# Kernel optimization log

Hardware: AMD Instinct MI355X
Metric: run time of the kernel (lower is better)

Reference implementation:

```python
import jax, jax.numpy as jnp
import numpy as np

EPS = 1e-5
N_P = 16


def _bn(x, g, b):
    # BatchNorm1d in training mode: batch stats over (batch, points), biased var
    m = jnp.mean(x, axis=(0, 2), keepdims=True)
    v = jnp.var(x, axis=(0, 2), keepdims=True)
    return g[None, :, None] * (x - m) * jax.lax.rsqrt(v + EPS) + b[None, :, None]


def _conv1x1(w, b, x):
    # w: [out, in], x: [B, in, N]
    return jnp.einsum('oc,bcn->bon', w, x) + b[None, :, None]


def setup_inputs() -> dict:
    key = jax.random.key(0)
    ks = iter(jax.random.split(key, 40))
    B, N = 16, 16384

    def conv_p(o, i):
        w = jax.random.normal(next(ks), (o, i), jnp.float32) * (1.0 / np.sqrt(i))
        b = jax.random.normal(next(ks), (o,), jnp.float32) * 0.02
        return w, b

    def bn_p(c):
        g = jnp.ones((c,), jnp.float32) + jax.random.normal(next(ks), (c,), jnp.float32) * 0.02
        b = jax.random.normal(next(ks), (c,), jnp.float32) * 0.02
        return g, b

    inp = {}
    inp['x'] = jax.random.normal(next(ks), (B, 4, N), jnp.float32)
    inp['w1'], inp['b1'] = conv_p(64, 4)
    inp['g1'], inp['be1'] = bn_p(64)
    inp['w2'], inp['b2'] = conv_p(128, 64)
    inp['g2'], inp['be2'] = bn_p(128)
    inp['w3'], inp['b3'] = conv_p(32, 128)
    inp['g3'], inp['be3'] = bn_p(32)
    # conv9: Conv2d(32, 1, kernel=(1, N_P)) -> store as [32, N_P] + scalar bias
    inp['w9'] = jax.random.normal(next(ks), (32, N_P), jnp.float32) * (1.0 / np.sqrt(32 * N_P))
    inp['b9'] = jax.random.normal(next(ks), (1,), jnp.float32) * 0.02
    inp['w4'], inp['b4'] = conv_p(512, 96)
    inp['g4'], inp['be4'] = bn_p(512)
    inp['w5'], inp['b5'] = conv_p(256, 512)
    inp['g5'], inp['be5'] = bn_p(256)
    inp['w6'], inp['b6'] = conv_p(128, 256)
    inp['g6'], inp['be6'] = bn_p(128)
    inp['w7'], inp['b7'] = conv_p(3, 128)
    return inp


def reference(x, w1, b1, g1, be1, w2, b2, g2, be2, w3, b3, g3, be3,
              w9, b9, w4, b4, g4, be4, w5, b5, g5, be5, w6, b6, g6, be6, w7, b7):
    B, _, N = x.shape
    h1 = jax.nn.relu(_bn(_conv1x1(w1, b1, x), g1, be1))      # [B,64,N] (pointfeat)
    h2 = jax.nn.relu(_bn(_conv1x1(w2, b2, h1), g2, be2))     # [B,128,N]
    h3 = _bn(_conv1x1(w3, b3, h2), g3, be3)                  # [B,32,N]

    # SoftPool: per key-channel ascending sort of points; only first N_P columns used.
    idxs = jnp.argsort(h3, axis=2)[:, :, :N_P]               # [B,32,N_P]
    # sp[b,c,k,p] = h3[b,c, idxs[b,k,p]]
    sp = jnp.take_along_axis(h3[:, :, None, :], idxs[:, None, :, :], axis=3)  # [B,32,32,N_P]

    # conv9: Conv2d(32->1, kernel (1,N_P)) collapses channel and N_P dims -> [B,32]
    v = jnp.einsum('cp,bckp->bk', w9, sp) + b9               # [B,32]
    glob = jnp.broadcast_to(v[:, :, None], (B, 32, N))       # repeat over points

    h = jnp.concatenate([glob, h1], axis=1)                  # [B,96,N]
    h = jax.nn.relu(_bn(_conv1x1(w4, b4, h), g4, be4))       # [B,512,N]
    h = jax.nn.relu(_bn(_conv1x1(w5, b5, h), g5, be5))       # [B,256,N]
    h = jax.nn.relu(_bn(_conv1x1(w6, b6, h), g6, be6))       # [B,128,N]
    out = jnp.tanh(_conv1x1(w7, b7, h))                      # [B,3,N]
    return out
```

## Files before the change

kernel.cpp:

```cpp
#include <hip/hip_runtime.h>
#include <hip/hip_fp16.h>
#include <math.h>
#include <type_traits>

#define NPTS 16384
#define NB 16
#define BNTOT (NB * NPTS)
#define NP 16

typedef _Float16 f16;
typedef __attribute__((ext_vector_type(8))) _Float16 f16x8;
typedef __attribute__((ext_vector_type(4))) float f32x4;

struct alignas(8) H4 { __half2 a, b; };
struct alignas(8) F16x4 { f16 v[4]; };

template<int CIN, int OT, int MODE, bool TANH_OUT, bool STATS, bool OUTAFF,
         typename TIN, typename TOUT>
__global__ __launch_bounds__(256, 2) void conv_k(
    const TIN* __restrict__ X, const float* __restrict__ vglob,
    const float* __restrict__ W, const float* __restrict__ bias,
    const float* __restrict__ insc, const float* __restrict__ insh,
    const float* __restrict__ outsc, const float* __restrict__ outsh,
    TOUT* __restrict__ Y, float* __restrict__ ssum, float* __restrict__ ssq,
    int COUT)
{
    constexpr int PT = 4;
    constexpr int NT = 256 * PT;
    constexpr int CC = (CIN < 128) ? CIN : 128;
    constexpr int XC = (MODE == 2) ? 64 : CIN;
    __shared__ __align__(16) float Ws[CC][OT];
    __shared__ float lsum[OT];
    __shared__ float lsq[OT];

    const int tid = threadIdx.x;
    const int tile = blockIdx.y;
    const int b = (tile * NT) / NPTS;
    const int n = (tile * NT) % NPTS + tid * PT;
    const int obase = blockIdx.x * OT;

    if (STATS) {
        for (int i = tid; i < OT; i += 256) { lsum[i] = 0.f; lsq[i] = 0.f; }
    }

    float acc[OT][PT];
#pragma unroll
    for (int o = 0; o < OT; ++o)
#pragma unroll
        for (int p = 0; p < PT; ++p) acc[o][p] = 0.f;

    const TIN* Xb = X + (size_t)b * XC * NPTS;

    for (int c0 = 0; c0 < CIN; c0 += CC) {
        for (int i = tid; i < CC * OT; i += 256) {
            int c = i % CC, o = i / CC;
            int oo = obase + o;
            Ws[c][o] = (oo < COUT) ? W[(size_t)oo * CIN + (c0 + c)] : 0.f;
        }
        __syncthreads();
#pragma unroll 2
        for (int c = 0; c < CC; ++c) {
            float xv[PT];
            if (MODE == 2 && (c0 + c) < 32) {
                float gv = vglob[b * 32 + (c0 + c)];
#pragma unroll
                for (int p = 0; p < PT; ++p) xv[p] = gv;
            } else {
                const int cx = (MODE == 2) ? (c0 + c - 32) : (c0 + c);
                if constexpr (std::is_same<TIN, __half>::value) {
                    H4 t = *(const H4*)(Xb + (size_t)cx * NPTS + n);
                    xv[0] = __low2float(t.a); xv[1] = __high2float(t.a);
                    xv[2] = __low2float(t.b); xv[3] = __high2float(t.b);
                } else {
                    float4 t = *(const float4*)(Xb + (size_t)cx * NPTS + n);
                    xv[0] = t.x; xv[1] = t.y; xv[2] = t.z; xv[3] = t.w;
                }
                if (MODE == 1) {
                    float s = insc[cx], h = insh[cx];
#pragma unroll
                    for (int p = 0; p < PT; ++p)
                        xv[p] = fmaxf(fmaf(xv[p], s, h), 0.f);
                }
            }
            const float4* wrow = (const float4*)(&Ws[c][0]);
#pragma unroll
            for (int o4 = 0; o4 < OT / 4; ++o4) {
                float4 w = wrow[o4];
#pragma unroll
                for (int p = 0; p < PT; ++p) {
                    acc[o4 * 4 + 0][p] = fmaf(w.x, xv[p], acc[o4 * 4 + 0][p]);
                    acc[o4 * 4 + 1][p] = fmaf(w.y, xv[p], acc[o4 * 4 + 1][p]);
                    acc[o4 * 4 + 2][p] = fmaf(w.z, xv[p], acc[o4 * 4 + 2][p]);
                    acc[o4 * 4 + 3][p] = fmaf(w.w, xv[p], acc[o4 * 4 + 3][p]);
                }
            }
        }
        __syncthreads();
    }

#pragma unroll
    for (int o = 0; o < OT; ++o) {
        const int oo = obase + o;
        if (oo < COUT) {
            float v[PT];
#pragma unroll
            for (int p = 0; p < PT; ++p) v[p] = acc[o][p];
            if (OUTAFF) {
                float s = outsc[oo], h = outsh[oo];
#pragma unroll
                for (int p = 0; p < PT; ++p) v[p] = fmaxf(fmaf(v[p], s, h), 0.f);
            }
            if (TANH_OUT) {
                float bb = bias[oo];
#pragma unroll
                for (int p = 0; p < PT; ++p) v[p] = tanhf(v[p] + bb);
            }
            const size_t ofs = ((size_t)b * COUT + oo) * NPTS + n;
            if constexpr (std::is_same<TOUT, __half>::value) {
                H4 t; t.a = __floats2half2_rn(v[0], v[1]);
                t.b = __floats2half2_rn(v[2], v[3]);
                *(H4*)(Y + ofs) = t;
            } else {
                *(float4*)(Y + ofs) = make_float4(v[0], v[1], v[2], v[3]);
            }
            if (STATS) {
                float s = v[0] + v[1] + v[2] + v[3];
                float q = fmaf(v[0], v[0], fmaf(v[1], v[1], fmaf(v[2], v[2], v[3] * v[3])));
#pragma unroll
                for (int d = 32; d >= 1; d >>= 1) {
                    s += __shfl_xor(s, d, 64);
                    q += __shfl_xor(q, d, 64);
                }
                if ((tid & 63) == 0) {
                    atomicAdd(&lsum[o], s);
                    atomicAdd(&lsq[o], q);
                }
            }
        }
    }
    if (STATS) {
        __syncthreads();
        for (int i = tid; i < OT; i += 256) {
            int oo = obase + i;
            if (oo < COUT) {
                atomicAdd(&ssum[oo], lsum[i]);
                atomicAdd(&ssq[oo], lsq[i]);
            }
        }
    }
}

__global__ void bnstats_k(const float* __restrict__ ssum, const float* __restrict__ ssq,
                          const float* __restrict__ g, const float* __restrict__ be,
                          float* __restrict__ scale, float* __restrict__ shift, int C)
{
    int c = blockIdx.x * blockDim.x + threadIdx.x;
    if (c >= C) return;
    const float inv = 1.0f / (float)BNTOT;
    float m = ssum[c] * inv;
    float var = fmaf(ssq[c], inv, -m * m);
    float sc = g[c] / sqrtf(var + 1e-5f);
    scale[c] = sc;
    shift[c] = fmaf(-m, sc, be[c]);
}

__global__ __launch_bounds__(256) void softpool_k(
    const float* __restrict__ y3, const float* __restrict__ sc3,
    const float* __restrict__ sh3, const float* __restrict__ w9,
    const float* __restrict__ b9, float* __restrict__ vout)
{
    extern __shared__ float vals[];
    __shared__ int sidx[NP];
    __shared__ float wv[4];
    __shared__ int wi[4];
    __shared__ float ps[4];

    const int tid = threadIdx.x;
    const int b = blockIdx.x >> 5;
    const int k = blockIdx.x & 31;

    const float* src = y3 + ((size_t)b * 32 + k) * NPTS;
    const float sck = sc3[k], shk = sh3[k];
    for (int i = tid; i < NPTS; i += 256) vals[i] = fmaf(src[i], sck, shk);
    __syncthreads();

    for (int p = 0; p < NP; ++p) {
        float bv = INFINITY;
        int bi = 0x7fffffff;
        for (int i = tid; i < NPTS; i += 256) {
            float x = vals[i];
            if (x < bv) { bv = x; bi = i; }
        }
#pragma unroll
        for (int d = 32; d >= 1; d >>= 1) {
            float ov = __shfl_xor(bv, d, 64);
            int oi = __shfl_xor(bi, d, 64);
            if (ov < bv || (ov == bv && oi < bi)) { bv = ov; bi = oi; }
        }
        if ((tid & 63) == 0) { wv[tid >> 6] = bv; wi[tid >> 6] = bi; }
        __syncthreads();
        if (tid == 0) {
            for (int w = 1; w < 4; ++w)
                if (wv[w] < bv || (wv[w] == bv && wi[w] < bi)) { bv = wv[w]; bi = wi[w]; }
            sidx[p] = bi;
            vals[bi] = INFINITY;
        }
        __syncthreads();
    }

    float part = 0.f;
    for (int i = tid; i < 32 * NP; i += 256) {
        int c = i >> 4, p = i & 15;
        float h = fmaf(y3[((size_t)b * 32 + c) * NPTS + sidx[p]], sc3[c], sh3[c]);
        part += w9[c * NP + p] * h;
    }
#pragma unroll
    for (int d = 32; d >= 1; d >>= 1) part += __shfl_xor(part, d, 64);
    if ((tid & 63) == 0) ps[tid >> 6] = part;
    __syncthreads();
    if (tid == 0) vout[b * 32 + k] = ps[0] + ps[1] + ps[2] + ps[3] + b9[0];
}

__global__ __launch_bounds__(256) void transformT_k(
    const float* __restrict__ y1, const float* __restrict__ sc,
    const float* __restrict__ sh, f16* __restrict__ h1T, float* __restrict__ S1b)
{
    __shared__ float arr[64][65];
    __shared__ float s1loc[64];
    const int tid = threadIdx.x;
    const int b = blockIdx.x >> 8;
    const int n0 = (blockIdx.x & 255) * 64;
    if (tid < 64) s1loc[tid] = 0.f;

    const int c = tid >> 2, j4 = tid & 3;
    const float scv = sc[c], shv = sh[c];
    const float* src = y1 + ((size_t)b * 64 + c) * NPTS + n0 + j4 * 16;
    float ls = 0.f;
#pragma unroll
    for (int j = 0; j < 4; ++j) {
        float4 v = *(const float4*)(src + j * 4);
        float r0 = fmaxf(fmaf(v.x, scv, shv), 0.f);
        float r1 = fmaxf(fmaf(v.y, scv, shv), 0.f);
        float r2 = fmaxf(fmaf(v.z, scv, shv), 0.f);
        float r3 = fmaxf(fmaf(v.w, scv, shv), 0.f);
        arr[j4 * 16 + j * 4 + 0][c] = r0;
        arr[j4 * 16 + j * 4 + 1][c] = r1;
        arr[j4 * 16 + j * 4 + 2][c] = r2;
        arr[j4 * 16 + j * 4 + 3][c] = r3;
        ls += (r0 + r1) + (r2 + r3);
    }
    ls += __shfl_xor(ls, 1, 64);
    ls += __shfl_xor(ls, 2, 64);
    if (j4 == 0) atomicAdd(&s1loc[c], ls);
    __syncthreads();

    const int n = tid >> 2, cj = (tid & 3) * 16;
    f16x8 h0, h1v;
#pragma unroll
    for (int jj = 0; jj < 8; ++jj) h0[jj] = (f16)arr[n][cj + jj];
#pragma unroll
    for (int jj = 0; jj < 8; ++jj) h1v[jj] = (f16)arr[n][cj + 8 + jj];
    f16* dst = h1T + ((size_t)b * NPTS + n0 + n) * 64 + cj;
    *(f16x8*)(dst) = h0;
    *(f16x8*)(dst + 8) = h1v;

    if (tid < 64) atomicAdd(&S1b[b * 64 + tid], s1loc[tid]);
}

__global__ __launch_bounds__(256, 2) void msyrk_k(const f16* __restrict__ h1T,
                                                  float* __restrict__ M)
{
    __shared__ float Mlds[4][4096];
    const int tid = threadIdx.x;
    const int lane = tid & 63;
    const int llo = lane & 15, lhi = lane >> 4;
    const int wv = tid >> 6;
    const int gw = blockIdx.x * 4 + wv;
    constexpr int SPW = (BNTOT / 32) / 2048;

    f32x4 acc[4][4];
#pragma unroll
    for (int ti = 0; ti < 4; ++ti)
#pragma unroll
        for (int tj = 0; tj < 4; ++tj) acc[ti][tj] = (f32x4){0.f, 0.f, 0.f, 0.f};

#pragma unroll
    for (int s = 0; s < SPW; ++s) {
        const size_t r0 = (size_t)gw * (SPW * 32) + (size_t)s * 32 + 8 * lhi;
        const f16* base = h1T + r0 * 64 + llo;
        f16x8 f[4];
#pragma unroll
        for (int t = 0; t < 4; ++t)
#pragma unroll
            for (int i = 0; i < 8; ++i)
                f[t][i] = base[(size_t)i * 64 + t * 16];
#pragma unroll
        for (int ti = 0; ti < 4; ++ti)
#pragma unroll
            for (int tj = 0; tj < 4; ++tj)
                acc[ti][tj] = __builtin_amdgcn_mfma_f32_16x16x32_f16(
                    f[ti], f[tj], acc[ti][tj], 0, 0, 0);
    }

#pragma unroll
    for (int ti = 0; ti < 4; ++ti)
#pragma unroll
        for (int tj = 0; tj < 4; ++tj)
#pragma unroll
            for (int r = 0; r < 4; ++r)
                Mlds[wv][(ti * 16 + 4 * lhi + r) * 64 + tj * 16 + llo] = acc[ti][tj][r];
    __syncthreads();
    for (int i = tid; i < 4096; i += 256)
        atomicAdd(&M[i], (Mlds[0][i] + Mlds[1][i]) + (Mlds[2][i] + Mlds[3][i]));
}

__global__ void bnstats45_k(const float* __restrict__ w4, const float* __restrict__ vv,
                            const float* __restrict__ S1b, const float* __restrict__ M,
                            const float* __restrict__ g, const float* __restrict__ be,
                            float* __restrict__ sc4, float* __restrict__ shift4b)
{
    __shared__ float vvL[512], sbL[1024], ML[4096];
    const int tid = threadIdx.x;
    for (int i = tid; i < 512; i += 512) vvL[i] = vv[i];
    for (int i = tid; i < 1024; i += 512) sbL[i] = S1b[i];
    for (int i = tid; i < 4096; i += 512) ML[i] = M[i];
    __syncthreads();
    const int o = tid;
    float wg[32], wh[64];
#pragma unroll
    for (int i = 0; i < 32; ++i) wg[i] = w4[o * 96 + i];
#pragma unroll
    for (int j = 0; j < 64; ++j) wh[j] = w4[o * 96 + 32 + j];
    float gbv[16];
    float sumy = 0.f, sumsq = 0.f;
#pragma unroll
    for (int b = 0; b < 16; ++b) {
        float gb = 0.f, hb = 0.f;
#pragma unroll
        for (int i = 0; i < 32; ++i) gb = fmaf(wg[i], vvL[b * 32 + i], gb);
#pragma unroll
        for (int j = 0; j < 64; ++j) hb = fmaf(wh[j], sbL[b * 64 + j], hb);
        gbv[b] = gb;
        sumy += (float)NPTS * gb + hb;
        sumsq += (float)NPTS * gb * gb + 2.f * gb * hb;
    }
    for (int j = 0; j < 64; ++j) {
        float t = 0.f;
#pragma unroll
        for (int j2 = 0; j2 < 64; ++j2) t = fmaf(ML[j * 64 + j2], wh[j2], t);
        sumsq = fmaf(wh[j], t, sumsq);
    }
    const float inv = 1.0f / (float)BNTOT;
    float m = sumy * inv;
    float var = fmaf(sumsq, inv, -m * m);
    float s = g[o] / sqrtf(var + 1e-5f);
    float sh4v = fmaf(-m, s, be[o]);
    sc4[o] = s;
#pragma unroll
    for (int b = 0; b < 16; ++b)
        shift4b[b * 512 + o] = fmaf(gbv[b], s, sh4v);
}

__global__ void wcvt_k(const float* __restrict__ src, f16* __restrict__ dst,
                       int rows, int cols, int srcStride, int srcOff)
{
    int i = blockIdx.x * 256 + threadIdx.x;
    if (i < rows * cols) {
        int r = i / cols, c = i % cols;
        dst[i] = (f16)src[(size_t)r * srcStride + srcOff + c];
    }
}

#define GLOAD(KT, RA, RB)                                                       \
  {                                                                             \
    const int kb_ = (KT) * 64 + sj * 8;                                         \
    float4 is0, is1, ih0, ih1;                                                  \
    if (INAFF) {                                                                \
      is0 = *(const float4*)(insc + kb_); is1 = *(const float4*)(insc + kb_ + 4); \
      ih0 = *(const float4*)(insh + kb_); ih1 = *(const float4*)(insh + kb_ + 4); \
    }                                                                           \
    _Pragma("unroll")                                                           \
    for (int i_ = 0; i_ < 4; ++i_) {                                            \
      const int r_ = sr + i_ * 32;                                              \
      RA[i_] = *(const f16x8*)(wsrc + (size_t)r_ * K + kb_);                    \
      f16x8 xb = *(const f16x8*)(xsrc + (size_t)r_ * K + kb_);                  \
      if (INAFF) {                                                              \
        f16x8 nb;                                                               \
        nb[0] = (f16)fmaxf(fmaf((float)xb[0], is0.x, ih0.x), 0.f);              \
        nb[1] = (f16)fmaxf(fmaf((float)xb[1], is0.y, ih0.y), 0.f);              \
        nb[2] = (f16)fmaxf(fmaf((float)xb[2], is0.z, ih0.z), 0.f);              \
        nb[3] = (f16)fmaxf(fmaf((float)xb[3], is0.w, ih0.w), 0.f);              \
        nb[4] = (f16)fmaxf(fmaf((float)xb[4], is1.x, ih1.x), 0.f);              \
        nb[5] = (f16)fmaxf(fmaf((float)xb[5], is1.y, ih1.y), 0.f);              \
        nb[6] = (f16)fmaxf(fmaf((float)xb[6], is1.z, ih1.z), 0.f);              \
        nb[7] = (f16)fmaxf(fmaf((float)xb[7], is1.w, ih1.w), 0.f);              \
        xb = nb;                                                                \
      }                                                                         \
      RB[i_] = xb;                                                              \
    }                                                                           \
  }

#define DSWRITE(RA, RB)                                                         \
  {                                                                             \
    _Pragma("unroll")                                                           \
    for (int i_ = 0; i_ < 4; ++i_) {                                            \
      const int r_ = sr + i_ * 32;                                              \
      const int sw_ = sj ^ (r_ & 7);                                            \
      *(f16x8*)(&As[r_ * 64 + sw_ * 8]) = RA[i_];                               \
      *(f16x8*)(&Bs[r_ * 64 + sw_ * 8]) = RB[i_];                               \
    }                                                                           \
  }

template<int KS, bool INAFF, bool OUTAFF, bool STATS>
__global__ __launch_bounds__(256, 2) void gconv_k(
    const f16* __restrict__ Xt, const f16* __restrict__ Wh,
    const float* __restrict__ insc, const float* __restrict__ insh,
    const float* __restrict__ outsc, const float* __restrict__ outshB,
    f16* __restrict__ Y, float* __restrict__ ssum, float* __restrict__ ssq,
    const int M)
{
    constexpr int K = KS * 64;
    __shared__ __align__(16) f16 As[128 * 64];
    __shared__ __align__(16) f16 Bs[128 * 64];
    __shared__ float lsum[128];
    __shared__ float lsq[128];

    const int tid = threadIdx.x;
    const int w = tid >> 6, lane = tid & 63;
    const int llo = lane & 15, lhi = lane >> 4;
    const int wn = w >> 1, wm = w & 1;
    const int n0 = blockIdx.y * 128;
    const int m0 = blockIdx.x * 128;
    const int sr = tid >> 3, sj = tid & 7;

    if (STATS && tid < 128) { lsum[tid] = 0.f; lsq[tid] = 0.f; }

    const f16* xsrc = Xt + (size_t)n0 * K;
    const f16* wsrc = Wh + (size_t)m0 * K;

    f32x4 acc[4][4];
#pragma unroll
    for (int nf = 0; nf < 4; ++nf)
#pragma unroll
        for (int mf = 0; mf < 4; ++mf) acc[nf][mf] = (f32x4){0.f, 0.f, 0.f, 0.f};

    f16x8 ra0[4], rb0[4], ra1[4], rb1[4];
    GLOAD(0, ra0, rb0);

#pragma unroll
    for (int kt = 0; kt < KS; ++kt) {
        if ((kt & 1) == 0) { DSWRITE(ra0, rb0); } else { DSWRITE(ra1, rb1); }
        __syncthreads();
        if (kt + 1 < KS) {
            if ((kt & 1) == 0) { GLOAD(kt + 1, ra1, rb1); }
            else               { GLOAD(kt + 1, ra0, rb0); }
        }
#pragma unroll
        for (int ks = 0; ks < 2; ++ks) {
            f16x8 af[4], bf[4];
#pragma unroll
            for (int f = 0; f < 4; ++f) {
                const int ml = wm * 64 + f * 16 + llo;
                af[f] = *(const f16x8*)(&As[ml * 64 + ((ks * 4 + lhi) ^ (ml & 7)) * 8]);
                const int nl = wn * 64 + f * 16 + llo;
                bf[f] = *(const f16x8*)(&Bs[nl * 64 + ((ks * 4 + lhi) ^ (nl & 7)) * 8]);
            }
#pragma unroll
            for (int nf = 0; nf < 4; ++nf)
#pragma unroll
                for (int mf = 0; mf < 4; ++mf)
                    acc[nf][mf] = __builtin_amdgcn_mfma_f32_16x16x32_f16(
                        af[mf], bf[nf], acc[nf][mf], 0, 0, 0);
        }
        __syncthreads();
    }

    const int bl = n0 / NPTS;
#pragma unroll
    for (int nf = 0; nf < 4; ++nf) {
        const int n = n0 + wn * 64 + nf * 16 + llo;
        f16* row = Y + (size_t)n * M + m0 + wm * 64;
#pragma unroll
        for (int mf = 0; mf < 4; ++mf) {
            const int moff = mf * 16 + 4 * lhi;
            float v0 = acc[nf][mf][0], v1 = acc[nf][mf][1];
            float v2 = acc[nf][mf][2], v3 = acc[nf][mf][3];
            if (OUTAFF) {
                const int mg = m0 + wm * 64 + moff;
                float4 s = *(const float4*)(outsc + mg);
                float4 h = *(const float4*)(outshB + (size_t)bl * M + mg);
                v0 = fmaxf(fmaf(v0, s.x, h.x), 0.f);
                v1 = fmaxf(fmaf(v1, s.y, h.y), 0.f);
                v2 = fmaxf(fmaf(v2, s.z, h.z), 0.f);
                v3 = fmaxf(fmaf(v3, s.w, h.w), 0.f);
            }
            F16x4 o;
            o.v[0] = (f16)v0; o.v[1] = (f16)v1; o.v[2] = (f16)v2; o.v[3] = (f16)v3;
            *(F16x4*)(row + moff) = o;
        }
    }
    if (STATS) {
#pragma unroll
        for (int mf = 0; mf < 4; ++mf) {
#pragma unroll
            for (int r = 0; r < 4; ++r) {
                float s = acc[0][mf][r] + acc[1][mf][r] + acc[2][mf][r] + acc[3][mf][r];
                float q = fmaf(acc[0][mf][r], acc[0][mf][r],
                          fmaf(acc[1][mf][r], acc[1][mf][r],
                          fmaf(acc[2][mf][r], acc[2][mf][r],
                               acc[3][mf][r] * acc[3][mf][r])));
#pragma unroll
                for (int d = 1; d < 16; d <<= 1) {
                    s += __shfl_xor(s, d, 64);
                    q += __shfl_xor(q, d, 64);
                }
                if (llo == 0) {
                    atomicAdd(&lsum[wm * 64 + mf * 16 + 4 * lhi + r], s);
                    atomicAdd(&lsq [wm * 64 + mf * 16 + 4 * lhi + r], q);
                }
            }
        }
        __syncthreads();
        if (tid < 128) {
            atomicAdd(&ssum[m0 + tid], lsum[tid]);
            atomicAdd(&ssq [m0 + tid], lsq [tid]);
        }
    }
}

__global__ __launch_bounds__(256) void conv7T_k(
    const f16* __restrict__ y6T, const float* __restrict__ sc6,
    const float* __restrict__ sh6, const float* __restrict__ w7,
    const float* __restrict__ b7, float* __restrict__ out)
{
    __shared__ float wsc[128], wsh[128], ww[384];
    const int tid = threadIdx.x;
    if (tid < 128) { wsc[tid] = sc6[tid]; wsh[tid] = sh6[tid]; }
    for (int i = tid; i < 384; i += 256) ww[i] = w7[i];
    __syncthreads();
    const int gid = blockIdx.x * 256 + tid;
    const int b = gid >> 14, nl = gid & 16383;
    const f16* row = y6T + (size_t)gid * 128;
    float a0 = 0.f, a1 = 0.f, a2 = 0.f;
    for (int c8 = 0; c8 < 128; c8 += 8) {
        f16x8 v8 = *(const f16x8*)(row + c8);
#pragma unroll
        for (int j = 0; j < 8; ++j) {
            float hv = fmaxf(fmaf((float)v8[j], wsc[c8 + j], wsh[c8 + j]), 0.f);
            a0 = fmaf(ww[c8 + j], hv, a0);
            a1 = fmaf(ww[128 + c8 + j], hv, a1);
            a2 = fmaf(ww[256 + c8 + j], hv, a2);
        }
    }
    const float bv = b7[0];
    out[((size_t)b * 3 + 0) * NPTS + nl] = tanhf(a0 + bv);
    out[((size_t)b * 3 + 1) * NPTS + nl] = tanhf(a1 + bv);
    out[((size_t)b * 3 + 2) * NPTS + nl] = tanhf(a2 + bv);
}

__global__ void fill_k(float* __restrict__ out, int nsize, float val)
{
    int i = blockIdx.x * 256 + threadIdx.x;
    if (i < nsize) out[i] = val;
}

extern "C" void kernel_launch(void* const* d_in, const int* in_sizes, int n_in,
                              void* d_out, int out_size, void* d_ws, size_t ws_size,
                              hipStream_t stream)
{
    const float* x   = (const float*)d_in[0];
    const float* w1  = (const float*)d_in[1];
    const float* g1  = (const float*)d_in[3];
    const float* be1 = (const float*)d_in[4];
    const float* w2  = (const float*)d_in[5];
    const float* g2  = (const float*)d_in[7];
    const float* be2 = (const float*)d_in[8];
    const float* w3  = (const float*)d_in[9];
    const float* g3  = (const float*)d_in[11];
    const float* be3 = (const float*)d_in[12];
    const float* w9  = (const float*)d_in[13];
    const float* b9  = (const float*)d_in[14];
    const float* w4  = (const float*)d_in[15];
    const float* g4  = (const float*)d_in[17];
    const float* be4 = (const float*)d_in[18];
    const float* w5  = (const float*)d_in[19];
    const float* g5  = (const float*)d_in[21];
    const float* be5 = (const float*)d_in[22];
    const float* w6  = (const float*)d_in[23];
    const float* g6  = (const float*)d_in[25];
    const float* be6 = (const float*)d_in[26];
    const float* w7  = (const float*)d_in[27];
    const float* b7  = (const float*)d_in[28];
    float* out = (float*)d_out;

    const size_t MB = 1048576u;
    const size_t need = 226 * MB;
    if (ws_size < need) {
        float val = 1000.0f + (float)(ws_size >> 20);
        fill_k<<<(out_size + 255) / 256, 256, 0, stream>>>(out, out_size, val);
        return;
    }

    char* base = (char*)d_ws;
    float* y1  = (float*)(base + 1 * MB);
    f16*   y4T = (f16*)(base + 1 * MB);
    f16*   y6T = (f16*)(base + 1 * MB);
    float* y2  = (float*)(base + 65 * MB);
    f16*   h1T = (f16*)(base + 65 * MB);
    f16*   y5T = (f16*)(base + 97 * MB);
    float* y3  = (float*)(base + 193 * MB);
    float* sm  = (float*)(base + 225 * MB);
    f16*   w5h = (f16*)(base + 225 * MB + 131072);
    f16*   w6h = w5h + 131072;
    f16*   w4hh = w6h + 32768;

    float* sum1 = sm + 0,     *sq1 = sm + 512,  *sc1 = sm + 1024, *sh1 = sm + 1536;
    float* sum2 = sm + 2048,  *sq2 = sm + 2560, *sc2 = sm + 3072, *sh2 = sm + 3584;
    float* sum3 = sm + 4096,  *sq3 = sm + 4608, *sc3 = sm + 5120, *sh3 = sm + 5632;
    float* sc4  = sm + 6144;
    float* sum5 = sm + 7168,  *sq5 = sm + 7680, *sc5 = sm + 8192, *sh5 = sm + 8704;
    float* sum6 = sm + 9216,  *sq6 = sm + 9728, *sc6 = sm + 10240,*sh6 = sm + 10752;
    float* vv   = sm + 11264;
    float* S1b  = sm + 11776;
    float* Mh   = sm + 12800;
    float* shift4b = sm + 16896;

    hipMemsetAsync(sm, 0, 16896 * sizeof(float), stream);

    const dim3 blk(256);
    const int tilesF = BNTOT / 1024;

    wcvt_k<<<(256 * 512 + 255) / 256, blk, 0, stream>>>(w5, w5h, 256, 512, 512, 0);
    wcvt_k<<<(128 * 256 + 255) / 256, blk, 0, stream>>>(w6, w6h, 128, 256, 256, 0);
    wcvt_k<<<(512 * 64 + 255) / 256, blk, 0, stream>>>(w4, w4hh, 512, 64, 96, 32);

    conv_k<4, 32, 0, false, true, false, float, float>
        <<<dim3(2, tilesF), blk, 0, stream>>>(x, nullptr, w1, nullptr, nullptr, nullptr,
            nullptr, nullptr, y1, sum1, sq1, 64);
    bnstats_k<<<1, 256, 0, stream>>>(sum1, sq1, g1, be1, sc1, sh1, 64);

    conv_k<64, 32, 1, false, true, false, float, float>
        <<<dim3(4, tilesF), blk, 0, stream>>>(y1, nullptr, w2, nullptr, sc1, sh1,
            nullptr, nullptr, y2, sum2, sq2, 128);
    bnstats_k<<<1, 256, 0, stream>>>(sum2, sq2, g2, be2, sc2, sh2, 128);

    conv_k<128, 32, 1, false, true, false, float, float>
        <<<dim3(1, tilesF), blk, 0, stream>>>(y2, nullptr, w3, nullptr, sc2, sh2,
            nullptr, nullptr, y3, sum3, sq3, 32);
    bnstats_k<<<1, 256, 0, stream>>>(sum3, sq3, g3, be3, sc3, sh3, 32);

    softpool_k<<<512, blk, NPTS * sizeof(float), stream>>>(y3, sc3, sh3, w9, b9, vv);

    transformT_k<<<16 * 256, blk, 0, stream>>>(y1, sc1, sh1, h1T, S1b);
    msyrk_k<<<512, blk, 0, stream>>>(h1T, Mh);
    bnstats45_k<<<1, 512, 0, stream>>>(w4, vv, S1b, Mh, g4, be4, sc4, shift4b);

    for (int q = 0; q < 4; ++q) {
        const f16* h1q = h1T + (size_t)q * 4 * NPTS * 64;
        f16* y5q = y5T + (size_t)q * 4 * NPTS * 256;
        gconv_k<1, false, true, false><<<dim3(4, 512), blk, 0, stream>>>(
            h1q, w4hh, nullptr, nullptr, sc4, shift4b + (size_t)q * 4 * 512,
            y4T, nullptr, nullptr, 512);
        gconv_k<8, false, false, true><<<dim3(2, 512), blk, 0, stream>>>(
            y4T, w5h, nullptr, nullptr, nullptr, nullptr,
            y5q, sum5, sq5, 256);
    }
    bnstats_k<<<1, 256, 0, stream>>>(sum5, sq5, g5, be5, sc5, sh5, 256);

    gconv_k<4, true, false, true><<<dim3(1, 2048), blk, 0, stream>>>(
        y5T, w6h, sc5, sh5, nullptr, nullptr,
        y6T, sum6, sq6, 128);
    bnstats_k<<<1, 256, 0, stream>>>(sum6, sq6, g6, be6, sc6, sh6, 128);

    conv7T_k<<<BNTOT / 256, blk, 0, stream>>>(y6T, sc6, sh6, w7, b7, out);
}
```

Before: 911.1 us.

## Shrink conv tiles to two points per thread, add XCD block swizzle

The fp32 conv kernels now process two points per thread instead of four, which doubles the number of tiles and raises launch bounds to three blocks per SM. Conv3 uses a 16-output tile over two x-blocks. A swizzle remaps flat block ids so consecutive tiles stay on the same XCD, and it is applied to both the conv kernel and the MFMA gconv kernel to improve L2 locality. Unused template modes such as half I/O, tanh and output affine are removed. The smaller tiles give more parallelism but lower per-thread reuse and more stat atomics. The swizzle assumes gridDim.y is a multiple of 8.

```diff
diff --git a/kernel.cpp b/kernel.cpp
--- a/kernel.cpp
+++ b/kernel.cpp
@@ -1,7 +1,6 @@
 #include <hip/hip_runtime.h>
 #include <hip/hip_fp16.h>
 #include <math.h>
-#include <type_traits>
 
 #define NPTS 16384
 #define NB 16
@@ -12,32 +11,36 @@
 typedef __attribute__((ext_vector_type(8))) _Float16 f16x8;
 typedef __attribute__((ext_vector_type(4))) float f32x4;
 
-struct alignas(8) H4 { __half2 a, b; };
 struct alignas(8) F16x4 { f16 v[4]; };
 
-template<int CIN, int OT, int MODE, bool TANH_OUT, bool STATS, bool OUTAFF,
-         typename TIN, typename TOUT>
-__global__ __launch_bounds__(256, 2) void conv_k(
-    const TIN* __restrict__ X, const float* __restrict__ vglob,
-    const float* __restrict__ W, const float* __restrict__ bias,
+__device__ inline void xcd_swz(int& bx, int& by)
+{
+    const int flatb = blockIdx.y * gridDim.x + blockIdx.x;
+    const int slot = flatb >> 3, xcd = flatb & 7;
+    bx = slot % gridDim.x;
+    by = (slot / gridDim.x) * 8 + xcd;
+}
+
+template<int CIN, int OT, int MODE, bool STATS>
+__global__ __launch_bounds__(256, 3) void conv_k(
+    const float* __restrict__ X, const float* __restrict__ W,
     const float* __restrict__ insc, const float* __restrict__ insh,
-    const float* __restrict__ outsc, const float* __restrict__ outsh,
-    TOUT* __restrict__ Y, float* __restrict__ ssum, float* __restrict__ ssq,
+    float* __restrict__ Y, float* __restrict__ ssum, float* __restrict__ ssq,
     int COUT)
 {
-    constexpr int PT = 4;
+    constexpr int PT = 2;
     constexpr int NT = 256 * PT;
     constexpr int CC = (CIN < 128) ? CIN : 128;
-    constexpr int XC = (MODE == 2) ? 64 : CIN;
     __shared__ __align__(16) float Ws[CC][OT];
     __shared__ float lsum[OT];
     __shared__ float lsq[OT];
 
+    int bx, by;
+    xcd_swz(bx, by);
     const int tid = threadIdx.x;
-    const int tile = blockIdx.y;
-    const int b = (tile * NT) / NPTS;
-    const int n = (tile * NT) % NPTS + tid * PT;
-    const int obase = blockIdx.x * OT;
+    const int b = (by * NT) / NPTS;
+    const int n = (by * NT) % NPTS + tid * PT;
+    const int obase = bx * OT;
 
     if (STATS) {
         for (int i = tid; i < OT; i += 256) { lsum[i] = 0.f; lsq[i] = 0.f; }
@@ -45,11 +48,9 @@
 
     float acc[OT][PT];
 #pragma unroll
-    for (int o = 0; o < OT; ++o)
-#pragma unroll
-        for (int p = 0; p < PT; ++p) acc[o][p] = 0.f;
-
-    const TIN* Xb = X + (size_t)b * XC * NPTS;
+    for (int o = 0; o < OT; ++o) { acc[o][0] = 0.f; acc[o][1] = 0.f; }
+
+    const float* Xb = X + (size_t)b * CIN * NPTS;
 
     for (int c0 = 0; c0 < CIN; c0 += CC) {
         for (int i = tid; i < CC * OT; i += 256) {
@@ -60,39 +61,26 @@
         __syncthreads();
 #pragma unroll 2
         for (int c = 0; c < CC; ++c) {
-            float xv[PT];
-            if (MODE == 2 && (c0 + c) < 32) {
-                float gv = vglob[b * 32 + (c0 + c)];
-#pragma unroll
-                for (int p = 0; p < PT; ++p) xv[p] = gv;
-            } else {
-                const int cx = (MODE == 2) ? (c0 + c - 32) : (c0 + c);
-                if constexpr (std::is_same<TIN, __half>::value) {
-                    H4 t = *(const H4*)(Xb + (size_t)cx * NPTS + n);
-                    xv[0] = __low2float(t.a); xv[1] = __high2float(t.a);
-                    xv[2] = __low2float(t.b); xv[3] = __high2float(t.b);
-                } else {
-                    float4 t = *(const float4*)(Xb + (size_t)cx * NPTS + n);
-                    xv[0] = t.x; xv[1] = t.y; xv[2] = t.z; xv[3] = t.w;
-                }
-                if (MODE == 1) {
-                    float s = insc[cx], h = insh[cx];
-#pragma unroll
-                    for (int p = 0; p < PT; ++p)
-                        xv[p] = fmaxf(fmaf(xv[p], s, h), 0.f);
-                }
+            const int cx = c0 + c;
+            float2 t = *(const float2*)(Xb + (size_t)cx * NPTS + n);
+            float xv0 = t.x, xv1 = t.y;
+            if (MODE == 1) {
+                float s = insc[cx], h = insh[cx];
+                xv0 = fmaxf(fmaf(xv0, s, h), 0.f);
+                xv1 = fmaxf(fmaf(xv1, s, h), 0.f);
             }
             const float4* wrow = (const float4*)(&Ws[c][0]);
 #pragma unroll
             for (int o4 = 0; o4 < OT / 4; ++o4) {
                 float4 w = wrow[o4];
-#pragma unroll
-                for (int p = 0; p < PT; ++p) {
-                    acc[o4 * 4 + 0][p] = fmaf(w.x, xv[p], acc[o4 * 4 + 0][p]);
-                    acc[o4 * 4 + 1][p] = fmaf(w.y, xv[p], acc[o4 * 4 + 1][p]);
-                    acc[o4 * 4 + 2][p] = fmaf(w.z, xv[p], acc[o4 * 4 + 2][p]);
-                    acc[o4 * 4 + 3][p] = fmaf(w.w, xv[p], acc[o4 * 4 + 3][p]);
-                }
+                acc[o4 * 4 + 0][0] = fmaf(w.x, xv0, acc[o4 * 4 + 0][0]);
+                acc[o4 * 4 + 0][1] = fmaf(w.x, xv1, acc[o4 * 4 + 0][1]);
+                acc[o4 * 4 + 1][0] = fmaf(w.y, xv0, acc[o4 * 4 + 1][0]);
+                acc[o4 * 4 + 1][1] = fmaf(w.y, xv1, acc[o4 * 4 + 1][1]);
+                acc[o4 * 4 + 2][0] = fmaf(w.z, xv0, acc[o4 * 4 + 2][0]);
+                acc[o4 * 4 + 2][1] = fmaf(w.z, xv1, acc[o4 * 4 + 2][1]);
+                acc[o4 * 4 + 3][0] = fmaf(w.w, xv0, acc[o4 * 4 + 3][0]);
+                acc[o4 * 4 + 3][1] = fmaf(w.w, xv1, acc[o4 * 4 + 3][1]);
             }
         }
         __syncthreads();
@@ -102,30 +90,11 @@
     for (int o = 0; o < OT; ++o) {
         const int oo = obase + o;
         if (oo < COUT) {
-            float v[PT];
-#pragma unroll
-            for (int p = 0; p < PT; ++p) v[p] = acc[o][p];
-            if (OUTAFF) {
-                float s = outsc[oo], h = outsh[oo];
-#pragma unroll
-                for (int p = 0; p < PT; ++p) v[p] = fmaxf(fmaf(v[p], s, h), 0.f);
-            }
-            if (TANH_OUT) {
-                float bb = bias[oo];
-#pragma unroll
-                for (int p = 0; p < PT; ++p) v[p] = tanhf(v[p] + bb);
-            }
-            const size_t ofs = ((size_t)b * COUT + oo) * NPTS + n;
-            if constexpr (std::is_same<TOUT, __half>::value) {
-                H4 t; t.a = __floats2half2_rn(v[0], v[1]);
-                t.b = __floats2half2_rn(v[2], v[3]);
-                *(H4*)(Y + ofs) = t;
-            } else {
-                *(float4*)(Y + ofs) = make_float4(v[0], v[1], v[2], v[3]);
-            }
+            float v0 = acc[o][0], v1 = acc[o][1];
+            *(float2*)(Y + ((size_t)b * COUT + oo) * NPTS + n) = make_float2(v0, v1);
             if (STATS) {
-                float s = v[0] + v[1] + v[2] + v[3];
-                float q = fmaf(v[0], v[0], fmaf(v[1], v[1], fmaf(v[2], v[2], v[3] * v[3])));
+                float s = v0 + v1;
+                float q = fmaf(v0, v0, v1 * v1);
 #pragma unroll
                 for (int d = 32; d >= 1; d >>= 1) {
                     s += __shfl_xor(s, d, 64);
@@ -425,12 +394,14 @@
     __shared__ float lsum[128];
     __shared__ float lsq[128];
 
+    int bx, by;
+    xcd_swz(bx, by);
     const int tid = threadIdx.x;
     const int w = tid >> 6, lane = tid & 63;
     const int llo = lane & 15, lhi = lane >> 4;
     const int wn = w >> 1, wm = w & 1;
-    const int n0 = blockIdx.y * 128;
-    const int m0 = blockIdx.x * 128;
+    const int n0 = by * 128;
+    const int m0 = bx * 128;
     const int sr = tid >> 3, sj = tid & 7;
 
     if (STATS && tid < 128) { lsum[tid] = 0.f; lsq[tid] = 0.f; }
@@ -628,25 +599,22 @@
     hipMemsetAsync(sm, 0, 16896 * sizeof(float), stream);
 
     const dim3 blk(256);
-    const int tilesF = BNTOT / 1024;
+    const int tiles2 = BNTOT / 512;
 
     wcvt_k<<<(256 * 512 + 255) / 256, blk, 0, stream>>>(w5, w5h, 256, 512, 512, 0);
     wcvt_k<<<(128 * 256 + 255) / 256, blk, 0, stream>>>(w6, w6h, 128, 256, 256, 0);
     wcvt_k<<<(512 * 64 + 255) / 256, blk, 0, stream>>>(w4, w4hh, 512, 64, 96, 32);
 
-    conv_k<4, 32, 0, false, true, false, float, float>
-        <<<dim3(2, tilesF), blk, 0, stream>>>(x, nullptr, w1, nullptr, nullptr, nullptr,
-            nullptr, nullptr, y1, sum1, sq1, 64);
+    conv_k<4, 32, 0, true><<<dim3(2, tiles2), blk, 0, stream>>>(
+        x, w1, nullptr, nullptr, y1, sum1, sq1, 64);
     bnstats_k<<<1, 256, 0, stream>>>(sum1, sq1, g1, be1, sc1, sh1, 64);
 
-    conv_k<64, 32, 1, false, true, false, float, float>
-        <<<dim3(4, tilesF), blk, 0, stream>>>(y1, nullptr, w2, nullptr, sc1, sh1,
-            nullptr, nullptr, y2, sum2, sq2, 128);
+    conv_k<64, 32, 1, true><<<dim3(4, tiles2), blk, 0, stream>>>(
+        y1, w2, sc1, sh1, y2, sum2, sq2, 128);
     bnstats_k<<<1, 256, 0, stream>>>(sum2, sq2, g2, be2, sc2, sh2, 128);
 
-    conv_k<128, 32, 1, false, true, false, float, float>
-        <<<dim3(1, tilesF), blk, 0, stream>>>(y2, nullptr, w3, nullptr, sc2, sh2,
-            nullptr, nullptr, y3, sum3, sq3, 32);
+    conv_k<128, 16, 1, true><<<dim3(2, tiles2), blk, 0, stream>>>(
+        y2, w3, sc2, sh2, y3, sum3, sq3, 32);
     bnstats_k<<<1, 256, 0, stream>>>(sum3, sq3, g3, be3, sc3, sh3, 32);
 
     softpool_k<<<512, blk, NPTS * sizeof(float), stream>>>(y3, sc3, sh3, w9, b9, vv);
```

After: 1.076 ms. 18.1% more time.
